# Kernel tuning notes

Measured on AMD Instinct MI355X. Metric: run time of the kernel, lower is better.

The kernel has to match this reference:

```python
import jax, jax.numpy as jnp
import numpy as np

B, N, C = 4, 4096, 1024
H, M = 16, 64          # num_heads, num_landmarks
DH = C // H
SCALE = H ** (-0.5)    # faithful to source: num_heads**-0.5
LN_EPS = 1e-5


def setup_inputs() -> dict:
    key = jax.random.key(0)
    ks = jax.random.split(key, 8)
    s = 0.02
    return {
        "x": jax.random.normal(ks[0], (B, N, C), jnp.float32),
        "ln_w": jnp.ones((C,), jnp.float32),
        "ln_b": jnp.zeros((C,), jnp.float32),
        "qkv_w": jax.random.normal(ks[1], (3 * C, C), jnp.float32) * s,
        "qkv_b": jax.random.normal(ks[2], (3 * C,), jnp.float32) * s,
        "gamma_w": jax.random.normal(ks[3], (C, C), jnp.float32) * s,
        "gamma_b": jax.random.normal(ks[4], (C,), jnp.float32) * s,
        "proj_w": jax.random.normal(ks[5], (C, C), jnp.float32) * s,
        "proj_b": jax.random.normal(ks[6], (C,), jnp.float32) * s,
    }


def _iterative_inv(K, n_iter=6):
    # Newton-Schulz pseudo-inverse on [..., M, M]
    Id = jnp.eye(K.shape[-1], dtype=K.dtype)
    KA = jnp.abs(K)
    V0 = KA.sum(axis=-2, keepdims=True).max(axis=-1, keepdims=True)
    VI = KA.sum(axis=-1, keepdims=True).max(axis=-2, keepdims=True)
    V = jnp.swapaxes(K, -2, -1) / (V0 * VI)
    for _ in range(n_iter):
        KV = K @ V
        V = 0.25 * V @ (13.0 * Id - KV @ (15.0 * Id - KV @ (7.0 * Id - KV)))
    return V


def reference(x, ln_w, ln_b, qkv_w, qkv_b, gamma_w, gamma_b, proj_w, proj_b):
    # LayerNorm
    mu = x.mean(axis=-1, keepdims=True)
    var = x.var(axis=-1, keepdims=True)
    xn = (x - mu) * jax.lax.rsqrt(var + LN_EPS) * ln_w + ln_b
    # qkv: (B,N,3C) -> (3,B,H,N,DH)
    qkv = (xn @ qkv_w.T + qkv_b).reshape(B, N, 3, H, DH).transpose(2, 0, 3, 1, 4)
    q, k, v = qkv[0], qkv[1], qkv[2]
    # landmarks: mean-pool segments of length N//M, then scale
    q_lm = q.reshape(B, H, M, N // M, DH).mean(axis=-2) * SCALE  # (B,H,M,DH)
    k_lm = k.reshape(B, H, M, N // M, DH).mean(axis=-2) * SCALE
    attn1 = jax.nn.softmax(jnp.einsum('bhnd,bhmd->bhnm', q, k_lm), axis=-1)    # (B,H,N,M)
    attn2 = jax.nn.softmax(jnp.einsum('bhmd,bhld->bhml', q_lm, k_lm), axis=-1)  # (B,H,M,M)
    attn3 = jax.nn.softmax(jnp.einsum('bhmd,bhnd->bhmn', q_lm, k), axis=-1)    # (B,H,M,N)
    attn2_inv = _iterative_inv(attn2)
    out = attn1 @ (attn2_inv @ (attn3 @ v))            # (B,H,N,DH)
    out = out.transpose(0, 2, 1, 3).reshape(B, N, C)
    out = out @ gamma_w.T + gamma_b                    # LipNorm=True branch
    out = out @ proj_w.T + proj_b                      # proj (dropout p=0 is identity)
    return out
```

## Files before the change

kernel.cpp:

```cpp
#include <hip/hip_runtime.h>
#include <stdint.h>

typedef unsigned short u16;
typedef short bf16x8 __attribute__((ext_vector_type(8)));
typedef float f32x4 __attribute__((ext_vector_type(4)));

#define MFMA16(a, b, c) __builtin_amdgcn_mfma_f32_16x16x32_bf16((a), (b), (c), 0, 0, 0)

static __device__ __forceinline__ float bfu2f(u16 u) {
  union { unsigned int i; float f; } z; z.i = ((unsigned int)u) << 16; return z.f;
}
static __device__ __forceinline__ u16 f2bfu(float f) {
  union { float f; unsigned int i; } z; z.f = f;
  unsigned int i = z.i;
  return (u16)((i + 0x7fffu + ((i >> 16) & 1u)) >> 16);
}

__device__ __forceinline__ void gload_lds16(const void* g, void* l) {
  __builtin_amdgcn_global_load_lds((const __attribute__((address_space(1))) void*)g,
                                   (__attribute__((address_space(3))) void*)l, 16, 0, 0);
}

__global__ __launch_bounds__(256) void ln_kernel(
    const float* __restrict__ x, const float* __restrict__ w,
    const float* __restrict__ b, u16* __restrict__ xn) {
  int row = blockIdx.x;
  int t = threadIdx.x;
  const float4* xr = (const float4*)(x + (size_t)row * 1024);
  float4 v = xr[t];
  float s = v.x + v.y + v.z + v.w;
  float ss = v.x * v.x + v.y * v.y + v.z * v.z + v.w * v.w;
#pragma unroll
  for (int m = 1; m < 64; m <<= 1) { s += __shfl_xor(s, m); ss += __shfl_xor(ss, m); }
  __shared__ float sb[4], ssb[4];
  int lane = t & 63, wvi = t >> 6;
  if (lane == 0) { sb[wvi] = s; ssb[wvi] = ss; }
  __syncthreads();
  s = sb[0] + sb[1] + sb[2] + sb[3];
  ss = ssb[0] + ssb[1] + ssb[2] + ssb[3];
  float mu = s * (1.0f / 1024.0f);
  float var = ss * (1.0f / 1024.0f) - mu * mu;
  float rstd = rsqrtf(var + 1e-5f);
  float4 wv4 = ((const float4*)w)[t];
  float4 bv4 = ((const float4*)b)[t];
  ushort4 o;
  o.x = f2bfu((v.x - mu) * rstd * wv4.x + bv4.x);
  o.y = f2bfu((v.y - mu) * rstd * wv4.y + bv4.y);
  o.z = f2bfu((v.z - mu) * rstd * wv4.z + bv4.z);
  o.w = f2bfu((v.w - mu) * rstd * wv4.w + bv4.w);
  ((ushort4*)xn)[(size_t)row * 256 + t] = o;
}

__global__ void cvt3_kernel(const float* __restrict__ a, u16* __restrict__ oa, int na,
                            const float* __restrict__ b, u16* __restrict__ ob, int nb,
                            const float* __restrict__ c, u16* __restrict__ oc, int nc) {
  int total = (na + nb + nc) >> 2;
  for (int i = blockIdx.x * blockDim.x + threadIdx.x; i < total; i += gridDim.x * blockDim.x) {
    int j = i << 2;
    const float* s; u16* d; int off;
    if (j < na) { s = a; d = oa; off = j; }
    else if (j < na + nb) { s = b; d = ob; off = j - na; }
    else { s = c; d = oc; off = j - na - nb; }
    float4 v = *(const float4*)(s + off);
    ushort4 o;
    o.x = f2bfu(v.x); o.y = f2bfu(v.y); o.z = f2bfu(v.z); o.w = f2bfu(v.w);
    *(ushort4*)(d + off) = o;
  }
}

template <int MODE>
__global__ __launch_bounds__(512, 2) void gemm_bt(
    const u16* __restrict__ A, const u16* __restrict__ Bw,
    const float* __restrict__ bias,
    float* __restrict__ Cf, u16* __restrict__ Cb,
    u16* __restrict__ Qo, u16* __restrict__ Ko, u16* __restrict__ Vo,
    int M, int N, int K) {
  __shared__ __attribute__((aligned(16))) u16 As[2][16384];
  __shared__ __attribute__((aligned(16))) u16 Bs[2][16384];
  int tid = threadIdx.x;
  int lane = tid & 63;
  int w = tid >> 6;
  int wr = w >> 2, wc = w & 3;
  int r16 = lane & 15, hi = lane >> 4;
  int l8 = lane >> 3, li = lane & 7;

  int nwg = gridDim.x * gridDim.y;
  int flat = blockIdx.y * gridDim.x + blockIdx.x;
  int q8 = nwg >> 3;
  int swz = (flat & 7) * q8 + (flat >> 3);
  int bx = swz % gridDim.x, by = swz / gridDim.x;

  const char* Abase = (const char*)(A + (size_t)by * 256 * K);
  const char* Bbase = (const char*)(Bw + (size_t)bx * 256 * K);
  size_t rowbytes = (size_t)K * 2;
  int colsw = (li ^ l8) << 4;
  int nkt = K >> 6;

  f32x4 z4 = {0.f, 0.f, 0.f, 0.f};
  f32x4 acc[8][4];
#pragma unroll
  for (int m = 0; m < 8; ++m)
#pragma unroll
    for (int n = 0; n < 4; ++n) acc[m][n] = z4;

#define SG_A(buf, t, r0)                                                      \
  gload_lds16(Abase + (size_t)((r0) + w * 8 + l8) * rowbytes + ((t) << 7) +   \
                  colsw,                                                      \
              (char*)As[buf] + ((r0) + w * 8) * 128)
#define SG_B(buf, t, r0)                                                      \
  gload_lds16(Bbase + (size_t)((r0) + w * 8 + l8) * rowbytes + ((t) << 7) +   \
                  colsw,                                                      \
              (char*)Bs[buf] + ((r0) + w * 8) * 128)

  SG_A(0, 0, 0); SG_A(0, 0, 64); SG_A(0, 0, 128); SG_A(0, 0, 192);
  SG_B(0, 0, 0); SG_B(0, 0, 64); SG_B(0, 0, 128); SG_B(0, 0, 192);
  SG_A(1, 1, 0); SG_A(1, 1, 128); SG_B(1, 1, 0); SG_B(1, 1, 64);
  SG_A(1, 1, 64); SG_A(1, 1, 192);
  asm volatile("s_waitcnt vmcnt(6)" ::: "memory");
  __builtin_amdgcn_s_barrier();
  __builtin_amdgcn_sched_barrier(0);

  int buf = 0;
  bf16x8 af[4][2], bfr[4][2];

#define LDA(mh)                                                               \
  _Pragma("unroll") for (int m = 0; m < 4; ++m) {                             \
    int row = wr * 128 + (mh) * 64 + m * 16 + r16;                            \
    int sw = (row & 7) << 4;                                                  \
    _Pragma("unroll") for (int kk = 0; kk < 2; ++kk)                          \
        af[m][kk] = *(const bf16x8*)(ab + row * 128 +                         \
                                     (((kk << 6) | (hi << 4)) ^ sw));         \
  }
#define LDB(nh)                                                               \
  _Pragma("unroll") for (int n = 0; n < 2; ++n) {                             \
    int row = wc * 64 + (nh) * 32 + n * 16 + r16;                             \
    int sw = (row & 7) << 4;                                                  \
    _Pragma("unroll") for (int kk = 0; kk < 2; ++kk)                          \
        bfr[(nh) * 2 + n][kk] = *(const bf16x8*)(ab2 + row * 128 +            \
                                     (((kk << 6) | (hi << 4)) ^ sw));         \
  }
#define MM(mh, nh)                                                            \
  __builtin_amdgcn_s_setprio(1);                                              \
  _Pragma("unroll") for (int kk = 0; kk < 2; ++kk)                            \
      _Pragma("unroll") for (int m = 0; m < 4; ++m)                           \
          _Pragma("unroll") for (int n = 0; n < 2; ++n)                       \
              acc[(mh) * 4 + m][(nh) * 2 + n] =                               \
      MFMA16(af[m][kk], bfr[(nh) * 2 + n][kk], acc[(mh) * 4 + m][(nh) * 2 + n]); \
  __builtin_amdgcn_s_setprio(0)

#define BAR1                                                                  \
  __builtin_amdgcn_s_barrier();                                               \
  __builtin_amdgcn_sched_barrier(0)
#define BAR2                                                                  \
  __builtin_amdgcn_sched_barrier(0);                                          \
  __builtin_amdgcn_s_barrier();                                               \
  __builtin_amdgcn_sched_barrier(0)

  for (int t = 0; t < nkt; ++t) {
    const char* ab = (const char*)As[buf];
    const char* ab2 = (const char*)Bs[buf];
    bool s1 = (t + 1 < nkt), s2 = (t + 2 < nkt);
    LDA(0);
    LDB(0);
    if (s1) { SG_B(buf ^ 1, t + 1, 128); SG_B(buf ^ 1, t + 1, 192); }
    BAR1;
    MM(0, 0);
    BAR2;
    LDB(1);
    if (s2) { SG_A(buf, t + 2, 0); SG_A(buf, t + 2, 128); }
    BAR1;
    MM(0, 1);
    BAR2;
    LDA(1);
    if (s2) { SG_B(buf, t + 2, 0); SG_B(buf, t + 2, 64); }
    BAR1;
    MM(1, 0);
    BAR2;
    if (s2) { SG_A(buf, t + 2, 64); SG_A(buf, t + 2, 192); }
    BAR1;
    MM(1, 1);
    __builtin_amdgcn_sched_barrier(0);
    if (s2) {
      asm volatile("s_waitcnt vmcnt(6)" ::: "memory");
    } else {
      asm volatile("s_waitcnt vmcnt(0)" ::: "memory");
    }
    __builtin_amdgcn_s_barrier();
    __builtin_amdgcn_sched_barrier(0);
    buf ^= 1;
  }
#undef SG_A
#undef SG_B
#undef LDA
#undef LDB
#undef MM
#undef BAR1
#undef BAR2

#pragma unroll
  for (int m = 0; m < 8; ++m)
#pragma unroll
    for (int n = 0; n < 4; ++n) {
      int row0 = by * 256 + wr * 128 + m * 16 + hi * 4;
      int col = bx * 256 + wc * 64 + n * 16 + r16;
      if (MODE == 2) {
        int jt = col >> 10;
        int h = (col >> 6) & 15, dh = col & 63;
        int bb = row0 >> 12, nt0 = row0 & 4095;
        float bcol = bias[col];
        if (jt == 2) {
          ushort4 o;
          o.x = f2bfu(acc[m][n][0] + bcol);
          o.y = f2bfu(acc[m][n][1] + bcol);
          o.z = f2bfu(acc[m][n][2] + bcol);
          o.w = f2bfu(acc[m][n][3] + bcol);
          *(ushort4*)&Vo[(((size_t)bb * 16 + h) * 64 + dh) * 4096 + nt0] = o;
        } else {
          u16* dst = (jt == 0) ? Qo : Ko;
#pragma unroll
          for (int r = 0; r < 4; ++r)
            dst[(((size_t)bb * 16 + h) * 4096 + nt0 + r) * 64 + dh] =
                f2bfu(acc[m][n][r] + bcol);
        }
      } else {
        float bcol = bias[col];
#pragma unroll
        for (int r = 0; r < 4; ++r) {
          int row = row0 + r;
          float val = acc[m][n][r] + bcol;
          if (MODE == 0) Cb[(size_t)row * N + col] = f2bfu(val);
          else           Cf[(size_t)row * N + col] = val;
        }
      }
    }
}

__global__ __launch_bounds__(64) void landmark_kernel(
    const u16* __restrict__ Q, const u16* __restrict__ K,
    float* __restrict__ qlmf, u16* __restrict__ qlmb,
    float* __restrict__ klmf, u16* __restrict__ klmb) {
  int bm = blockIdx.x;
  int bh = bm >> 6, m = bm & 63;
  int d = threadIdx.x;
  const u16* src = blockIdx.y ? K : Q;
  const u16* p = src + (((size_t)bh * 4096) + m * 64) * 64 + d;
  float s = 0.f;
#pragma unroll 8
  for (int r = 0; r < 64; ++r) s += bfu2f(p[(size_t)r * 64]);
  float val = s * (0.25f / 64.0f);
  size_t o = (size_t)bh * 4096 + m * 64 + d;
  if (blockIdx.y) { klmf[o] = val; klmb[o] = f2bfu(val); }
  else            { qlmf[o] = val; qlmb[o] = f2bfu(val); }
}

__global__ __launch_bounds__(256) void attn3_pv_kernel(
    const u16* __restrict__ qlmb, const u16* __restrict__ Kmat,
    const u16* __restrict__ Vt, float* __restrict__ Upart,
    float* __restrict__ rspart) {
  __shared__ __attribute__((aligned(16))) u16 Elds[4][8192];
  int chunk = blockIdx.x, bh = blockIdx.y;
  int tid = threadIdx.x, lane = tid & 63, w = tid >> 6;
  int r16 = lane & 15, hi = lane >> 4;
  int keybase = chunk * 512 + w * 128;
  const u16* kb = Kmat + ((size_t)bh * 4096 + keybase) * 64;
  const u16* vtb = Vt + (size_t)bh * 262144;
  const u16* qb = qlmb + (size_t)bh * 4096;
  u16* eb = &Elds[w][0];
  f32x4 z4 = {0.f, 0.f, 0.f, 0.f};

  bf16x8 afr[4][2];
#pragma unroll
  for (int m = 0; m < 4; ++m)
#pragma unroll
    for (int kk = 0; kk < 2; ++kk)
      afr[m][kk] = *(const bf16x8*)(qb + (m * 16 + r16) * 64 + kk * 32 + hi * 8);

  float rs[4][4] = {};
  for (int cf = 0; cf < 8; ++cf) {
    f32x4 S[4] = {z4, z4, z4, z4};
#pragma unroll
    for (int kk = 0; kk < 2; ++kk) {
      bf16x8 bfr = *(const bf16x8*)(kb + (size_t)(cf * 16 + r16) * 64 + kk * 32 + hi * 8);
#pragma unroll
      for (int m = 0; m < 4; ++m) S[m] = MFMA16(afr[m][kk], bfr, S[m]);
    }
#pragma unroll
    for (int m = 0; m < 4; ++m)
#pragma unroll
      for (int r = 0; r < 4; ++r) {
        float e = __expf(S[m][r]);
        rs[m][r] += e;
        int row = m * 16 + hi * 4 + r;
        int key = cf * 16 + r16;
        *(u16*)((char*)eb + row * 256 + ((key * 2) ^ ((row & 7) << 4))) = f2bfu(e);
      }
  }
#pragma unroll
  for (int m = 0; m < 4; ++m)
#pragma unroll
    for (int r = 0; r < 4; ++r) {
      float v = rs[m][r];
      v += __shfl_xor(v, 1); v += __shfl_xor(v, 2);
      v += __shfl_xor(v, 4); v += __shfl_xor(v, 8);
      rs[m][r] = v;
    }
  if (r16 == 0) {
    float* rp = rspart + (((size_t)bh * 8 + chunk) * 4 + w) * 64;
#pragma unroll
    for (int m = 0; m < 4; ++m)
#pragma unroll
      for (int r = 0; r < 4; ++r) rp[m * 16 + hi * 4 + r] = rs[m][r];
  }
  __syncthreads();

  f32x4 U[4][4];
#pragma unroll
  for (int m = 0; m < 4; ++m)
#pragma unroll
    for (int df = 0; df < 4; ++df) U[m][df] = z4;
  for (int ks = 0; ks < 4; ++ks) {
    bf16x8 ea[4];
#pragma unroll
    for (int m = 0; m < 4; ++m) {
      int row = m * 16 + r16;
      ea[m] = *(const bf16x8*)((char*)eb + row * 256 + (((ks * 32 + hi * 8) * 2) ^ ((row & 7) << 4)));
    }
#pragma unroll
    for (int df = 0; df < 4; ++df) {
      bf16x8 vb8 = *(const bf16x8*)(vtb + (size_t)(df * 16 + r16) * 4096 +
                                    keybase + ks * 32 + hi * 8);
#pragma unroll
      for (int m = 0; m < 4; ++m) U[m][df] = MFMA16(ea[m], vb8, U[m][df]);
    }
  }
  float* up = Upart + (((size_t)bh * 8 + chunk) * 4 + w) * 4096;
#pragma unroll
  for (int m = 0; m < 4; ++m)
#pragma unroll
    for (int df = 0; df < 4; ++df)
#pragma unroll
      for (int r = 0; r < 4; ++r)
        up[(m * 16 + hi * 4 + r) * 64 + df * 16 + r16] = U[m][df][r];
}

__global__ __launch_bounds__(256) void reduce_t_kernel(
    const float* __restrict__ Upart, const float* __restrict__ rspart,
    float* __restrict__ Tmf) {
  int bh = blockIdx.y;
  int tid = threadIdx.x;
  __shared__ float rsum[64];
  if (tid < 64) {
    float s = 0.f;
    const float* rp = rspart + (size_t)bh * 2048 + tid;
#pragma unroll 8
    for (int p = 0; p < 32; ++p) s += rp[p * 64];
    rsum[tid] = s;
  }
  __syncthreads();
  int idx4 = blockIdx.x * 256 + tid;
  const float4* up = (const float4*)(Upart + (size_t)bh * 131072) + idx4;
  float4 s = {0.f, 0.f, 0.f, 0.f};
#pragma unroll 8
  for (int p = 0; p < 32; ++p) {
    float4 v = up[p * 1024];
    s.x += v.x; s.y += v.y; s.z += v.z; s.w += v.w;
  }
  float inv = 1.0f / rsum[idx4 >> 4];
  s.x *= inv; s.y *= inv; s.z *= inv; s.w *= inv;
  ((float4*)(Tmf + (size_t)bh * 4096))[idx4] = s;
}

__device__ __forceinline__ void mm64(const float (*AT)[68], const float (*Bm)[68],
                                     float (*C)[68], float (*CT)[68],
                                     float alpha, int tid) {
  int tr = (tid >> 4) << 2;
  int tc = (tid & 15) << 2;
  float acc[4][4] = {};
#pragma unroll 4
  for (int k = 0; k < 64; ++k) {
    float4 av = *(const float4*)&AT[k][tr];
    float4 bv = *(const float4*)&Bm[k][tc];
    float aa[4] = {av.x, av.y, av.z, av.w};
    float bb[4] = {bv.x, bv.y, bv.z, bv.w};
#pragma unroll
    for (int i = 0; i < 4; ++i)
#pragma unroll
      for (int j = 0; j < 4; ++j) acc[i][j] = fmaf(aa[i], bb[j], acc[i][j]);
  }
#pragma unroll
  for (int i = 0; i < 4; ++i)
#pragma unroll
    for (int j = 0; j < 4; ++j) {
      float vv = acc[i][j] * alpha;
      C[tr + i][tc + j] = vv;
      if (CT) CT[tc + j][tr + i] = vv;
    }
}

__global__ __launch_bounds__(256) void combine_ns_kernel(
    const float* __restrict__ Tmf, const float* __restrict__ qlmf,
    const float* __restrict__ klmf, u16* __restrict__ WT) {
  __shared__ __attribute__((aligned(16))) float A2T[64][68];
  __shared__ __attribute__((aligned(16))) float Vv[64][68];
  __shared__ __attribute__((aligned(16))) float VT[64][68];
  __shared__ __attribute__((aligned(16))) float KV[64][68];
  __shared__ __attribute__((aligned(16))) float KVT[64][68];
  __shared__ __attribute__((aligned(16))) float T2[64][68];
  __shared__ __attribute__((aligned(16))) float T4[64][68];
  __shared__ __attribute__((aligned(16))) float Tm[64][68];
  __shared__ float redbuf[64];
  __shared__ float v0s, scal;
  int bh = blockIdx.x, tid = threadIdx.x;

  for (int idx = tid; idx < 1024; idx += 256) {
    float4 v = ((const float4*)(Tmf + (size_t)bh * 4096))[idx];
    int r = idx >> 4, c0 = (idx & 15) << 2;
    *(float4*)&Tm[r][c0] = v;
  }
  for (int idx = tid; idx < 4096; idx += 256) {
    int r = idx >> 6, c = idx & 63;
    Vv[c][r] = qlmf[(size_t)bh * 4096 + idx];
    VT[c][r] = klmf[(size_t)bh * 4096 + idx];
  }
  __syncthreads();
  mm64(&Vv[0], &VT[0], &T2[0], nullptr, 1.0f, tid);
  __syncthreads();
  if (tid < 64) {
    float mx = -1e30f;
    for (int c2 = 0; c2 < 64; ++c2) mx = fmaxf(mx, T2[tid][c2]);
    float s = 0.f;
    for (int c2 = 0; c2 < 64; ++c2) { float e = __expf(T2[tid][c2] - mx); T2[tid][c2] = e; s += e; }
    float inv = 1.f / s;
    for (int c2 = 0; c2 < 64; ++c2) { float p = T2[tid][c2] * inv; T2[tid][c2] = p; A2T[c2][tid] = p; }
  }
  __syncthreads();
  if (tid < 64) {
    float cs = 0.f;
    for (int r2 = 0; r2 < 64; ++r2) cs += fabsf(T2[r2][tid]);
    redbuf[tid] = cs;
  }
  __syncthreads();
  if (tid == 0) {
    float v0 = 0.f;
    for (int c2 = 0; c2 < 64; ++c2) v0 = fmaxf(v0, redbuf[c2]);
    v0s = v0;
  }
  __syncthreads();
  if (tid < 64) {
    float rs2 = 0.f;
    for (int c2 = 0; c2 < 64; ++c2) rs2 += fabsf(T2[tid][c2]);
    redbuf[tid] = rs2;
  }
  __syncthreads();
  if (tid == 0) {
    float vi = 0.f;
    for (int r2 = 0; r2 < 64; ++r2) vi = fmaxf(vi, redbuf[r2]);
    scal = 1.0f / (v0s * vi);
  }
  __syncthreads();
  for (int idx = tid; idx < 4096; idx += 256) {
    int r = idx >> 6, c = idx & 63;
    Vv[r][c] = A2T[r][c] * scal;
    VT[r][c] = T2[r][c] * scal;
  }
  __syncthreads();
#pragma unroll 1
  for (int it = 0; it < 6; ++it) {
    mm64(&A2T[0], &Vv[0], &KV[0], &KVT[0], 1.0f, tid);
    __syncthreads();
    for (int idx = tid; idx < 4096; idx += 256) {
      int r = idx >> 6, c = idx & 63;
      T2[r][c] = ((r == c) ? 7.0f : 0.0f) - KV[r][c];
    }
    __syncthreads();
    mm64(&KVT[0], &T2[0], &T4[0], nullptr, 1.0f, tid);
    __syncthreads();
    for (int idx = tid; idx < 4096; idx += 256) {
      int r = idx >> 6, c = idx & 63;
      T2[r][c] = ((r == c) ? 15.0f : 0.0f) - T4[r][c];
    }
    __syncthreads();
    mm64(&KVT[0], &T2[0], &T4[0], nullptr, 1.0f, tid);
    __syncthreads();
    for (int idx = tid; idx < 4096; idx += 256) {
      int r = idx >> 6, c = idx & 63;
      T2[r][c] = ((r == c) ? 13.0f : 0.0f) - T4[r][c];
    }
    __syncthreads();
    mm64(&VT[0], &T2[0], &T4[0], nullptr, 0.25f, tid);
    __syncthreads();
    for (int idx = tid; idx < 4096; idx += 256) {
      int r = idx >> 6, c = idx & 63;
      float vvv = T4[r][c];
      Vv[r][c] = vvv; VT[c][r] = vvv;
    }
    __syncthreads();
  }
  mm64(&VT[0], &Tm[0], &T2[0], nullptr, 1.0f, tid);
  __syncthreads();
  for (int idx = tid; idx < 4096; idx += 256) {
    int r = idx >> 6, c = idx & 63;
    WT[(size_t)bh * 4096 + c * 64 + r] = f2bfu(T2[r][c]);
  }
}

__global__ __launch_bounds__(256) void attn1_out_kernel(
    const u16* __restrict__ Q, const u16* __restrict__ klmb,
    const u16* __restrict__ WT, u16* __restrict__ AO) {
  __shared__ __attribute__((aligned(16))) u16 Elds[4][2048];
  int bh = blockIdx.y;
  int b = bh >> 4, h = bh & 15;
  int tid = threadIdx.x, lane = tid & 63, w = tid >> 6;
  int r16 = lane & 15, hi = lane >> 4;
  int rowbase = blockIdx.x * 128 + w * 32;
  const u16* qb = Q + ((size_t)bh * 4096 + rowbase) * 64;
  const u16* kb = klmb + (size_t)bh * 4096;
  const u16* wtb = WT + (size_t)bh * 4096;
  u16* eb = &Elds[w][0];
  f32x4 z4 = {0.f, 0.f, 0.f, 0.f};

  bf16x8 afr[2][2];
#pragma unroll
  for (int mi = 0; mi < 2; ++mi)
#pragma unroll
    for (int kk = 0; kk < 2; ++kk)
      afr[mi][kk] = *(const bf16x8*)(qb + (mi * 16 + r16) * 64 + kk * 32 + hi * 8);

  float rs[2][4] = {};
  for (int cf = 0; cf < 4; ++cf) {
    f32x4 S[2] = {z4, z4};
#pragma unroll
    for (int kk = 0; kk < 2; ++kk) {
      bf16x8 bfr = *(const bf16x8*)(kb + (cf * 16 + r16) * 64 + kk * 32 + hi * 8);
#pragma unroll
      for (int mi = 0; mi < 2; ++mi) S[mi] = MFMA16(afr[mi][kk], bfr, S[mi]);
    }
#pragma unroll
    for (int mi = 0; mi < 2; ++mi)
#pragma unroll
      for (int r = 0; r < 4; ++r) {
        float e = __expf(S[mi][r]);
        rs[mi][r] += e;
        int row = mi * 16 + hi * 4 + r;
        int key = cf * 16 + r16;
        *(u16*)((char*)eb + row * 128 + ((key * 2) ^ ((row & 7) << 4))) = f2bfu(e);
      }
  }
#pragma unroll
  for (int mi = 0; mi < 2; ++mi)
#pragma unroll
    for (int r = 0; r < 4; ++r) {
      float v = rs[mi][r];
      v += __shfl_xor(v, 1); v += __shfl_xor(v, 2);
      v += __shfl_xor(v, 4); v += __shfl_xor(v, 8);
      rs[mi][r] = v;
    }
  __syncthreads();

  f32x4 O[2][4];
#pragma unroll
  for (int mi = 0; mi < 2; ++mi)
#pragma unroll
    for (int df = 0; df < 4; ++df) O[mi][df] = z4;
  for (int ks = 0; ks < 2; ++ks) {
    bf16x8 ea[2];
#pragma unroll
    for (int mi = 0; mi < 2; ++mi) {
      int row = mi * 16 + r16;
      ea[mi] = *(const bf16x8*)((char*)eb + row * 128 + (((ks * 32 + hi * 8) * 2) ^ ((row & 7) << 4)));
    }
#pragma unroll
    for (int df = 0; df < 4; ++df) {
      bf16x8 wfr = *(const bf16x8*)(wtb + (df * 16 + r16) * 64 + ks * 32 + hi * 8);
#pragma unroll
      for (int mi = 0; mi < 2; ++mi) O[mi][df] = MFMA16(ea[mi], wfr, O[mi][df]);
    }
  }
#pragma unroll
  for (int mi = 0; mi < 2; ++mi)
#pragma unroll
    for (int df = 0; df < 4; ++df)
#pragma unroll
      for (int r = 0; r < 4; ++r) {
        int row = mi * 16 + hi * 4 + r;
        int n = rowbase + row;
        int col = h * 64 + df * 16 + r16;
        float val = O[mi][df][r] / rs[mi][r];
        AO[((size_t)b * 4096 + n) * 1024 + col] = f2bfu(val);
      }
}

extern "C" void kernel_launch(void* const* d_in, const int* in_sizes, int n_in,
                              void* d_out, int out_size, void* d_ws, size_t ws_size,
                              hipStream_t stream) {
  (void)in_sizes; (void)n_in; (void)out_size; (void)ws_size;
  const float* x       = (const float*)d_in[0];
  const float* ln_w    = (const float*)d_in[1];
  const float* ln_b    = (const float*)d_in[2];
  const float* qkv_w   = (const float*)d_in[3];
  const float* qkv_b   = (const float*)d_in[4];
  const float* gamma_w = (const float*)d_in[5];
  const float* gamma_b = (const float*)d_in[6];
  const float* proj_w  = (const float*)d_in[7];
  const float* proj_b  = (const float*)d_in[8];

  char* ws = (char*)d_ws;
  u16* XN     = (u16*)(ws + 0);
  u16* Qb     = (u16*)(ws + 33554432);
  u16* Kb     = (u16*)(ws + 67108864);
  u16* Vb     = (u16*)(ws + 100663296);
  u16* QKVW   = (u16*)(ws + 134217728);
  u16* GW     = (u16*)(ws + 140509184);
  u16* PW     = (u16*)(ws + 142606336);
  float* QLMF = (float*)(ws + 144703488);
  float* KLMF = (float*)(ws + 145752064);
  u16* QLMB   = (u16*)(ws + 146800640);
  u16* KLMB   = (u16*)(ws + 147324928);
  float* RSP  = (float*)(ws + 147849216);
  u16* WTb    = (u16*)(ws + 148373504);
  float* UP   = (float*)XN;
  float* TMF  = (float*)Kb;

  ln_kernel<<<16384, 256, 0, stream>>>(x, ln_w, ln_b, XN);
  cvt3_kernel<<<2048, 256, 0, stream>>>(qkv_w, QKVW, 3145728,
                                        gamma_w, GW, 1048576,
                                        proj_w, PW, 1048576);
  gemm_bt<2><<<dim3(12, 64), 512, 0, stream>>>(XN, QKVW, qkv_b, nullptr, nullptr,
                                               Qb, Kb, Vb, 16384, 3072, 1024);
  landmark_kernel<<<dim3(4096, 2), 64, 0, stream>>>(Qb, Kb, QLMF, QLMB, KLMF, KLMB);
  attn3_pv_kernel<<<dim3(8, 64), 256, 0, stream>>>(QLMB, Kb, Vb, UP, RSP);
  reduce_t_kernel<<<dim3(4, 64), 256, 0, stream>>>(UP, RSP, TMF);
  combine_ns_kernel<<<64, 256, 0, stream>>>(TMF, QLMF, KLMF, WTb);
  attn1_out_kernel<<<dim3(32, 64), 256, 0, stream>>>(Qb, KLMB, WTb, XN);
  gemm_bt<0><<<dim3(4, 64), 512, 0, stream>>>(XN, GW, gamma_b, nullptr, Kb,
                                              nullptr, nullptr, nullptr, 16384, 1024, 1024);
  gemm_bt<1><<<dim3(4, 64), 512, 0, stream>>>(Kb, PW, proj_b, (float*)d_out, nullptr,
                                              nullptr, nullptr, nullptr, 16384, 1024, 1024);
}
```

Measured before the change: 370.7 us.

## Fold gamma and proj linear layers into one precomputed weight GEMM

Merges the two back-to-back linear layers (gamma then proj) into a single 16384x1024x1024 GEMM. The combined weight proj_w·gamma_w is built by a small 1024^3 GEMM after transposing gamma_w, and the combined bias proj_w·gamma_b + proj_b by a separate kernel. This removes one large GEMM and its bf16 intermediate round-trip, at the cost of extra rounding in the merged bf16 weight and a few small setup kernels. The landmark mean-pooling kernel also switches to 16-byte vector loads with a shuffle reduction.

```diff
diff --git a/kernel.cpp b/kernel.cpp
--- a/kernel.cpp
+++ b/kernel.cpp
@@ -223,13 +223,14 @@
                 f2bfu(acc[m][n][r] + bcol);
         }
       } else {
-        float bcol = bias[col];
+        float bcol = 0.f;
+        if constexpr (MODE != 3) bcol = bias[col];
 #pragma unroll
         for (int r = 0; r < 4; ++r) {
           int row = row0 + r;
           float val = acc[m][n][r] + bcol;
-          if (MODE == 0) Cb[(size_t)row * N + col] = f2bfu(val);
-          else           Cf[(size_t)row * N + col] = val;
+          if (MODE == 1) Cf[(size_t)row * N + col] = val;
+          else           Cb[(size_t)row * N + col] = f2bfu(val);
         }
       }
     }
@@ -241,16 +242,35 @@
     float* __restrict__ klmf, u16* __restrict__ klmb) {
   int bm = blockIdx.x;
   int bh = bm >> 6, m = bm & 63;
-  int d = threadIdx.x;
+  int l = threadIdx.x;
   const u16* src = blockIdx.y ? K : Q;
-  const u16* p = src + (((size_t)bh * 4096) + m * 64) * 64 + d;
-  float s = 0.f;
-#pragma unroll 8
-  for (int r = 0; r < 64; ++r) s += bfu2f(p[(size_t)r * 64]);
-  float val = s * (0.25f / 64.0f);
-  size_t o = (size_t)bh * 4096 + m * 64 + d;
-  if (blockIdx.y) { klmf[o] = val; klmb[o] = f2bfu(val); }
-  else            { qlmf[o] = val; qlmb[o] = f2bfu(val); }
+  const u16* base = src + (((size_t)bh * 4096) + m * 64) * 64;
+  int r0 = l >> 3;
+  int c0 = (l & 7) * 8;
+  float s[8] = {};
+#pragma unroll
+  for (int p = 0; p < 8; ++p) {
+    bf16x8 v = *(const bf16x8*)(base + (size_t)(r0 + p * 8) * 64 + c0);
+#pragma unroll
+    for (int j = 0; j < 8; ++j) s[j] += bfu2f((u16)v[j]);
+  }
+#pragma unroll
+  for (int j = 0; j < 8; ++j) {
+    s[j] += __shfl_xor(s[j], 8);
+    s[j] += __shfl_xor(s[j], 16);
+    s[j] += __shfl_xor(s[j], 32);
+  }
+  if (l < 8) {
+    size_t o = (size_t)bh * 4096 + m * 64 + l * 8;
+    float* fo = blockIdx.y ? klmf : qlmf;
+    u16* bo = blockIdx.y ? klmb : qlmb;
+#pragma unroll
+    for (int j = 0; j < 8; ++j) {
+      float val = s[j] * (0.25f / 64.0f);
+      fo[o + j] = val;
+      bo[o + j] = f2bfu(val);
+    }
+  }
 }
 
 __global__ __launch_bounds__(256) void attn3_pv_kernel(
@@ -368,6 +388,32 @@
   float inv = 1.0f / rsum[idx4 >> 4];
   s.x *= inv; s.y *= inv; s.z *= inv; s.w *= inv;
   ((float4*)(Tmf + (size_t)bh * 4096))[idx4] = s;
+}
+
+__global__ __launch_bounds__(256) void transpose_g_kernel(
+    const float* __restrict__ G, u16* __restrict__ GT) {
+  __shared__ float t[64][65];
+  int tr = blockIdx.y * 64, tc = blockIdx.x * 64;
+  int l = threadIdx.x & 63, y = threadIdx.x >> 6;
+  for (int r = y; r < 64; r += 4)
+    t[r][l] = G[(size_t)(tr + r) * 1024 + tc + l];
+  __syncthreads();
+  for (int rr = y; rr < 64; rr += 4)
+    GT[(size_t)(tc + rr) * 1024 + tr + l] = f2bfu(t[l][rr]);
+}
+
+__global__ __launch_bounds__(256) void bias2_kernel(
+    const float* __restrict__ P, const float* __restrict__ gb,
+    const float* __restrict__ pb, float* __restrict__ b2) {
+  int i = blockIdx.x * 256 + threadIdx.x;
+  const float4* pr = (const float4*)(P + (size_t)i * 1024);
+  const float4* g4 = (const float4*)gb;
+  float s = 0.f;
+  for (int k = 0; k < 256; ++k) {
+    float4 a = pr[k], b = g4[k];
+    s += a.x * b.x + a.y * b.y + a.z * b.z + a.w * b.w;
+  }
+  b2[i] = s + pb[i];
 }
 
 __device__ __forceinline__ void mm64(const float (*AT)[68], const float (*Bm)[68],
@@ -620,6 +666,9 @@
   u16* WTb    = (u16*)(ws + 148373504);
   float* UP   = (float*)XN;
   float* TMF  = (float*)Kb;
+  u16* GTb    = (u16*)(ws + 100663296);
+  u16* W2b    = (u16*)(ws + 102760448);
+  float* B2F  = (float*)(ws + 104857600);
 
   ln_kernel<<<16384, 256, 0, stream>>>(x, ln_w, ln_b, XN);
   cvt3_kernel<<<2048, 256, 0, stream>>>(qkv_w, QKVW, 3145728,
@@ -630,10 +679,12 @@
   landmark_kernel<<<dim3(4096, 2), 64, 0, stream>>>(Qb, Kb, QLMF, QLMB, KLMF, KLMB);
   attn3_pv_kernel<<<dim3(8, 64), 256, 0, stream>>>(QLMB, Kb, Vb, UP, RSP);
   reduce_t_kernel<<<dim3(4, 64), 256, 0, stream>>>(UP, RSP, TMF);
+  transpose_g_kernel<<<dim3(16, 16), 256, 0, stream>>>(gamma_w, GTb);
+  gemm_bt<3><<<dim3(4, 4), 512, 0, stream>>>(PW, GTb, nullptr, nullptr, W2b,
+                                             nullptr, nullptr, nullptr, 1024, 1024, 1024);
+  bias2_kernel<<<4, 256, 0, stream>>>(proj_w, gamma_b, proj_b, B2F);
   combine_ns_kernel<<<64, 256, 0, stream>>>(TMF, QLMF, KLMF, WTb);
   attn1_out_kernel<<<dim3(32, 64), 256, 0, stream>>>(Qb, KLMB, WTb, XN);
-  gemm_bt<0><<<dim3(4, 64), 512, 0, stream>>>(XN, GW, gamma_b, nullptr, Kb,
+  gemm_bt<1><<<dim3(4, 64), 512, 0, stream>>>(XN, W2b, B2F, (float*)d_out, nullptr,
                                               nullptr, nullptr, nullptr, 16384, 1024, 1024);
-  gemm_bt<1><<<dim3(4, 64), 512, 0, stream>>>(Kb, PW, proj_b, (float*)d_out, nullptr,
-                                              nullptr, nullptr, nullptr, 16384, 1024, 1024);
-}
+}
```

After: 403.4 us. +8.8%, slower.
